# Kernel optimization log

Measured on AMD Instinct MI355X. Metric: run time of the kernel, lower is better.

The kernel has to match this reference:

```python
import jax, jax.numpy as jnp
import numpy as np
from jax import lax

N = 8192            # total ensemble boxes
W_IMG, H_IMG = 1920.0, 1080.0
NUM_MODELS = 5
CLUSTER_IOU = 0.5   # coalesce_boxes threshold


def setup_inputs() -> dict:
    key = jax.random.key(0)
    k1, k2, k3, k4, k5 = jax.random.split(key, 5)
    x1 = jax.random.uniform(k1, (N,)) * (W_IMG - 60.0)
    y1 = jax.random.uniform(k2, (N,)) * (H_IMG - 60.0)
    w = jax.random.uniform(k3, (N,)) * 180.0 + 4.0
    h = jax.random.uniform(k4, (N,)) * 180.0 + 4.0
    boxes = jnp.stack([x1, y1, x1 + w, y1 + h], axis=1)          # [N,4] xyxy
    scores = jax.random.uniform(k5, (N,)) * 0.7 + 0.3            # conf_thres=0.3
    return {"boxes": boxes, "scores": scores, "num_models": NUM_MODELS}


def _edf_forward(boxes, scores, num_models):
    n = boxes.shape[0]
    # clip to image (original also rounds; rounding omitted to keep grads alive)
    x1 = jnp.clip(boxes[:, 0], 0.0, W_IMG)
    y1 = jnp.clip(boxes[:, 1], 0.0, H_IMG)
    x2 = jnp.clip(boxes[:, 2], 0.0, W_IMG)
    y2 = jnp.clip(boxes[:, 3], 0.0, H_IMG)
    # coalesce_boxes processes boxes in descending score order (sort asc, pop)
    order = jnp.argsort(-scores)
    b = jnp.stack([x1, y1, x2, y2], axis=1)[order]               # [N,4]
    s = scores[order]
    bx1, by1, bx2, by2 = b[:, 0], b[:, 1], b[:, 2], b[:, 3]
    area = (bx2 - bx1 + 1.0) * (by2 - by1 + 1.0)
    # pairwise IoU with the +1 convention of bb_intersection_over_union
    ix1 = jnp.maximum(bx1[:, None], bx1[None, :])
    iy1 = jnp.maximum(by1[:, None], by1[None, :])
    ix2 = jnp.minimum(bx2[:, None], bx2[None, :])
    iy2 = jnp.minimum(by2[:, None], by2[None, :])
    inter = jnp.maximum(ix2 - ix1 + 1.0, 0.0) * jnp.maximum(iy2 - iy1 + 1.0, 0.0)
    iou = inter / (area[:, None] + area[None, :] - inter)        # [N,N]
    adj = iou > CLUSTER_IOU
    # greedy clustering: in score order, an unassigned box becomes a cluster
    # head and absorbs every still-unassigned box with IoU(head, j) > 0.5
    def step(cluster, i):
        is_head = cluster[i] < 0
        cluster = jnp.where(is_head & (cluster < 0) & adj[i], i, cluster)
        return cluster, None
    cluster, _ = lax.scan(step, jnp.full((n,), -1, jnp.int32),
                          jnp.arange(n, dtype=jnp.int32))
    counts = jax.ops.segment_sum(jnp.ones((n,), jnp.float32), cluster, num_segments=n)
    # per-group nms() only returns pick[0]: the member with max y2 (ties -> first)
    seg_y2 = jax.ops.segment_max(by2, cluster, num_segments=n)
    idx = jnp.arange(n)
    cand = by2 >= seg_y2[cluster]
    first = jax.ops.segment_min(jnp.where(cand, idx, n), cluster, num_segments=n)
    is_pick = idx == first[cluster]
    # probFinal = sum of group scores; final score = probFinal / num_models
    prob = jax.ops.segment_sum(s, cluster, num_segments=n)
    score_out = prob[cluster] / num_models
    # 'consensus': keep group iff its size >= num_models / 3
    valid = counts >= (num_models / 3.0)
    keep = is_pick & valid[cluster]
    out = jnp.where(keep[:, None],
                    jnp.concatenate([b, score_out[:, None]], axis=1),
                    0.0)                                         # [N,5] padded
    return out, keep


def reference(boxes, scores, num_models):
    return _edf_forward(boxes, scores, num_models)
```

## Files before the change

### kernel.cpp

```cpp
#include <hip/hip_runtime.h>
#include <cstdint>

#define N 8192
#define NT 128
#define NROUNDS 6
typedef unsigned long long u64;
typedef unsigned int u32;

__device__ inline u64 readlane64(u64 v, int lane) {
  u32 lo = (u32)__builtin_amdgcn_readlane((int)(u32)v, lane);
  u32 hi = (u32)__builtin_amdgcn_readlane((int)(u32)(v >> 32), lane);
  return ((u64)hi << 32) | lo;
}

__global__ __launch_bounds__(256) void k_rank0(const float* __restrict__ scores,
                                               const float* __restrict__ boxes,
                                               float* __restrict__ bx1s, float* __restrict__ by1s,
                                               float* __restrict__ bx2s, float* __restrict__ by2s,
                                               float* __restrict__ ss, float* __restrict__ areas,
                                               int* __restrict__ cnt,
                                               float* __restrict__ prob,
                                               u64* __restrict__ y2f,
                                               u64* __restrict__ D,
                                               u64* __restrict__ S) {
#pragma clang fp contract(off)
  __shared__ u64 tile[1024];
  __shared__ int red[8][32];
  int t = threadIdx.x;
  int s = t >> 5, ei = t & 31;
  int e = blockIdx.x * 32 + ei;
  u64 ke = ((u64)__float_as_uint(scores[e]) << 32) | (u32)(0xFFFFFFFFu - (u32)e);
  int c = 0;
  for (int j0 = 0; j0 < N; j0 += 1024) {
    __syncthreads();
    for (int q = t; q < 1024; q += 256) {
      int j = j0 + q;
      tile[q] = ((u64)__float_as_uint(scores[j]) << 32) | (u32)(0xFFFFFFFFu - (u32)j);
    }
    __syncthreads();
    int k0 = s * 128;
#pragma unroll 8
    for (int k = 0; k < 128; ++k) c += (tile[k0 + k] > ke) ? 1 : 0;
  }
  red[s][ei] = c;
  __syncthreads();
  if (t < 32) {
    int r = 0;
#pragma unroll
    for (int q = 0; q < 8; ++q) r += red[q][t];
    int i = blockIdx.x * 32 + t;
    float x1 = fminf(fmaxf(boxes[i * 4 + 0], 0.0f), 1920.0f);
    float y1 = fminf(fmaxf(boxes[i * 4 + 1], 0.0f), 1080.0f);
    float x2 = fminf(fmaxf(boxes[i * 4 + 2], 0.0f), 1920.0f);
    float y2 = fminf(fmaxf(boxes[i * 4 + 3], 0.0f), 1080.0f);
    bx1s[r] = x1; by1s[r] = y1; bx2s[r] = x2; by2s[r] = y2;
    ss[r] = scores[i];
    areas[r] = (x2 - x1 + 1.0f) * (y2 - y1 + 1.0f);
    cnt[i] = 0; prob[i] = 0.0f; y2f[i] = 0ull;
  }
  if (blockIdx.x == 0) {
    if (t < NT) D[t] = 0ull;
    else if (t < 2 * NT) S[t - NT] = 0ull;
  }
}

__global__ __launch_bounds__(256) void k_adj(const float* __restrict__ bx1s, const float* __restrict__ by1s,
                                             const float* __restrict__ bx2s, const float* __restrict__ by2s,
                                             const float* __restrict__ areas,
                                             u64* __restrict__ mtile) {
#pragma clang fp contract(off)
  __shared__ float jx1[4][64], jy1[4][64], jx2[4][64], jy2[4][64], ja[4][64];
  int w = threadIdx.x >> 6, l = threadIdx.x & 63;
  int p = blockIdx.x * 4 + w;
  int gy = (int)((sqrtf(8.0f * (float)p + 1.0f) - 1.0f) * 0.5f);
  while ((gy + 1) * (gy + 2) / 2 <= p) ++gy;
  while (gy * (gy + 1) / 2 > p) --gy;
  int gx = p - gy * (gy + 1) / 2;

  int j = gx * 64 + l;
  jx1[w][l] = bx1s[j]; jy1[w][l] = by1s[j]; jx2[w][l] = bx2s[j]; jy2[w][l] = by2s[j]; ja[w][l] = areas[j];
  __syncthreads();
  int i = gy * 64 + l;
  float x1 = bx1s[i], y1 = by1s[i], x2 = bx2s[i], y2 = by2s[i], ai = areas[i];
  u64 bits = 0;
#pragma unroll 4
  for (int jj = 0; jj < 64; ++jj) {
    float ix1 = fmaxf(x1, jx1[w][jj]);
    float iy1 = fmaxf(y1, jy1[w][jj]);
    float ix2 = fminf(x2, jx2[w][jj]);
    float iy2 = fminf(y2, jy2[w][jj]);
    float iw = fmaxf(ix2 - ix1 + 1.0f, 0.0f);
    float ih = fmaxf(iy2 - iy1 + 1.0f, 0.0f);
    float inter = iw * ih;
    float uni = (ai + ja[w][jj]) - inter;
    float t = inter + inter;
    bool gt = t > uni;
    bool amb = fabsf(t - uni) <= 1e-6f * uni;
    if (__ballot(amb) != 0ull) {
      float iou = inter / uni;
      if (amb) gt = iou > 0.5f;
    }
    bits |= ((u64)gt) << jj;
  }
  mtile[((size_t)gy * NT + gx) * 64 + l] = bits;
  if (gx != gy) {
    u64 tb = 0;
#pragma unroll 8
    for (int c = 0; c < 64; ++c) {
      u64 wb = __ballot((bits >> c) & 1ull);
      tb = (l == c) ? wb : tb;
    }
    mtile[((size_t)gx * NT + gy) * 64 + l] = tb;
  }
}

__global__ __launch_bounds__(256) void k_round(const u64* __restrict__ mtile,
                                               u64* __restrict__ D,
                                               u64* __restrict__ S) {
  __shared__ u64 Dl[NT], Sl[NT];
  __shared__ u64 bw[3][4];
  int gy = blockIdx.x;
  int t = threadIdx.x;
  int w = t >> 6, r = t & 63;
  if (t < NT) Dl[t] = D[t];
  else Sl[t - NT] = S[t - NT];
  __syncthreads();
  u64 classified = Dl[gy] | Sl[gy];
  if (classified == ~0ull) return;
  bool unk = !((classified >> r) & 1ull);
  u64 anyD = 0, anyU = 0, anyE = 0;
  if (unk) {
    int k0 = 32 * w, k1 = min(k0 + 32, gy + 1);
    for (int k = k0; k < k1; ++k) {
      u64 m = mtile[((size_t)gy * NT + k) * 64 + r];
      if (k == gy) {
        m &= (1ull << r) - 1ull;
        anyD |= m & Dl[k];
        anyU |= m & ~Sl[k];
      } else {
        anyD |= m & Dl[k];
        anyU |= m & ~Sl[k];
        anyE |= m & ~(Sl[k] | Dl[k]);
      }
    }
  }
  u64 bD = __ballot(anyD != 0ull), bU = __ballot(anyU != 0ull), bE = __ballot(anyE != 0ull);
  if (r == 0) { bw[0][w] = bD; bw[1][w] = bU; bw[2][w] = bE; }
  __syncthreads();
  u64 rD = bw[0][0] | bw[0][1] | bw[0][2] | bw[0][3];
  u64 rU = bw[1][0] | bw[1][1] | bw[1][2] | bw[1][3];
  u64 rE = bw[2][0] | bw[2][1] | bw[2][2] | bw[2][3];
  u64 unkb = ~classified;
  if (rE == 0ull) {
    if (w == 0) {
      u64 dAA = mtile[((size_t)gy * NT + gy) * 64 + r];
      u64 heads = 0, todo = unkb & ~rD;
      while (todo) {
        int i = __builtin_ctzll(todo);
        heads |= 1ull << i;
        todo &= ~readlane64(dAA, i);
      }
      if (r == 0) {
        if (heads) atomicOr(&D[gy], heads);
        u64 ns = unkb & ~heads;
        if (ns) atomicOr(&S[gy], ns);
      }
    }
    return;
  }
  if (t == 0) {
    u64 newS = unkb & rD;
    u64 newD = unkb & ~rD & ~rU;
    if (newS) atomicOr(&S[gy], newS);
    if (newD) atomicOr(&D[gy], newD);
  }
}

__global__ __launch_bounds__(64, 1) void k_fix(const u64* __restrict__ mtile,
                                               u64* __restrict__ D,
                                               const u64* __restrict__ S) {
  __shared__ int ulist[N];
  int l = threadIdx.x;
  u64 D0 = D[l], D1 = D[64 + l];
  u64 S0 = S[l], S1 = S[64 + l];
  u64 u0 = ~(D0 | S0), u1 = ~(D1 | S1);
  int c0 = __popcll(u0), c1 = __popcll(u1);
  int p0 = c0, p1 = c1;
  for (int d = 1; d < 64; d <<= 1) {
    int v0 = __shfl_up(p0, d), v1 = __shfl_up(p1, d);
    if (l >= d) { p0 += v0; p1 += v1; }
  }
  int t0 = __shfl(p0, 63);
  int M = t0 + __shfl(p1, 63);
  {
    int o = p0 - c0;
    u64 v = u0;
    while (v) { int b = __builtin_ctzll(v); v &= v - 1; ulist[o++] = l * 64 + b; }
    o = t0 + p1 - c1;
    v = u1;
    while (v) { int b = __builtin_ctzll(v); v &= v - 1; ulist[o++] = (64 + l) * 64 + b; }
  }
  __syncthreads();
  if (M > 0) {
    u64 rx[8], ry[8];
    int pj[8];
    auto fetch = [&](int q, int j) {
      pj[q] = j;
      int jt = j >> 6, jl = j & 63;
      rx[q] = mtile[((size_t)jt * NT + l) * 64 + jl];
      ry[q] = mtile[((size_t)jt * NT + 64 + l) * 64 + jl];
    };
#pragma unroll
    for (int q = 0; q < 8; ++q) fetch(q, ulist[q < M ? q : M - 1]);
    for (int m = 0; m < M; ++m) {
      int slot = m & 7;
      int j = pj[slot];
      u64 vx = rx[slot], vy = ry[slot];
      int jt = j >> 6;
      u64 bm = (1ull << (j & 63)) - 1ull;
      u64 m0 = (l < jt) ? ~0ull : ((l == jt) ? bm : 0ull);
      u64 m1 = (64 + l < jt) ? ~0ull : ((64 + l == jt) ? bm : 0ull);
      bool hit = ((vx & D0 & m0) | (vy & D1 & m1)) != 0ull;
      bool head = (__ballot(hit) == 0ull);
      u64 bset = 1ull << (j & 63);
      D0 |= (head && (l == jt)) ? bset : 0ull;
      D1 |= (head && (64 + l == jt)) ? bset : 0ull;
      int nm = m + 8;
      fetch(slot, ulist[nm < M ? nm : M - 1]);
    }
  }
  D[l] = D0;
  D[64 + l] = D1;
}

__global__ __launch_bounds__(256) void k_cluster(const u64* __restrict__ mtile,
                                                 const u64* __restrict__ D,
                                                 const float* __restrict__ ss,
                                                 const float* __restrict__ by2s,
                                                 int* __restrict__ cluster,
                                                 int* __restrict__ cnt,
                                                 float* __restrict__ prob,
                                                 u64* __restrict__ y2f) {
  __shared__ u64 hlds[NT];
  __shared__ int red[4][64];
  int gy = blockIdx.x;
  if (threadIdx.x < NT) hlds[threadIdx.x] = D[threadIdx.x];
  __syncthreads();
  int w = threadIdx.x >> 6, r = threadIdx.x & 63;
  int best = 0x7fffffff;
  for (int kk = 0; kk < 32; ++kk) {
    int k = 32 * w + kk;
    u64 v = mtile[((size_t)gy * NT + k) * 64 + r] & hlds[k];
    if (v && best == 0x7fffffff) best = k * 64 + __builtin_ctzll(v);
  }
  red[w][r] = best;
  __syncthreads();
  if (w == 0) {
    int b = min(min(red[0][r], red[1][r]), min(red[2][r], red[3][r]));
    int j = gy * 64 + r;
    cluster[j] = b;
    atomicAdd(&cnt[b], 1);
    atomicAdd(&prob[b], ss[j]);
    u64 key = ((u64)__float_as_uint(by2s[j]) << 32) | (u32)(0xFFFFFFFFu - (u32)j);
    atomicMax(&y2f[b], key);
  }
}

__global__ __launch_bounds__(256) void k_out(const int* __restrict__ cluster,
                                             const float* __restrict__ bx1s, const float* __restrict__ by1s,
                                             const float* __restrict__ bx2s, const float* __restrict__ by2s,
                                             const int* __restrict__ cnt,
                                             const float* __restrict__ prob,
                                             const u64* __restrict__ y2f,
                                             const int* __restrict__ num_models,
                                             float* __restrict__ out) {
  int j = blockIdx.x * 256 + threadIdx.x;
  if (j >= N) return;
  int c = cluster[j];
  int nm = num_models[0];
  bool valid = (float)cnt[c] >= (float)nm / 3.0f;
  int jf = (int)(0xFFFFFFFFu - (u32)(y2f[c] & 0xFFFFFFFFull));
  bool keep = (jf == j) && valid;
  float o0 = 0.f, o1 = 0.f, o2 = 0.f, o3 = 0.f, o4 = 0.f;
  if (keep) {
    o0 = bx1s[j]; o1 = by1s[j]; o2 = bx2s[j]; o3 = by2s[j];
    o4 = prob[c] / (float)nm;
  }
  out[j * 5 + 0] = o0;
  out[j * 5 + 1] = o1;
  out[j * 5 + 2] = o2;
  out[j * 5 + 3] = o3;
  out[j * 5 + 4] = o4;
  out[N * 5 + j] = keep ? 1.0f : 0.0f;
}

extern "C" void kernel_launch(void* const* d_in, const int* in_sizes, int n_in,
                              void* d_out, int out_size, void* d_ws, size_t ws_size,
                              hipStream_t stream) {
  const float* boxes = (const float*)d_in[0];
  const float* scores = (const float*)d_in[1];
  const int* num_models = (const int*)d_in[2];
  float* out = (float*)d_out;

  char* p = (char*)d_ws;
  auto take = [&](size_t bytes) {
    char* r = p;
    p += (bytes + 255) & ~(size_t)255;
    return r;
  };
  float* bx1s = (float*)take((size_t)N * 4);
  float* by1s = (float*)take((size_t)N * 4);
  float* bx2s = (float*)take((size_t)N * 4);
  float* by2s = (float*)take((size_t)N * 4);
  float* ss   = (float*)take((size_t)N * 4);
  float* areas= (float*)take((size_t)N * 4);
  int* cluster= (int*)take((size_t)N * 4);
  int* cnt    = (int*)take((size_t)N * 4);
  float* prob = (float*)take((size_t)N * 4);
  u64* y2f    = (u64*)take((size_t)N * 8);
  u64* D      = (u64*)take((size_t)NT * 8);
  u64* S      = (u64*)take((size_t)NT * 8);
  u64* mtile  = (u64*)take((size_t)NT * NT * 64 * 8);

  k_rank0<<<N / 32, 256, 0, stream>>>(scores, boxes, bx1s, by1s, bx2s, by2s, ss, areas,
                                      cnt, prob, y2f, D, S);
  k_adj<<<NT * (NT + 1) / 2 / 4, 256, 0, stream>>>(bx1s, by1s, bx2s, by2s, areas, mtile);
  for (int r = 0; r < NROUNDS; ++r)
    k_round<<<NT, 256, 0, stream>>>(mtile, D, S);
  k_fix<<<1, 64, 0, stream>>>(mtile, D, S);
  k_cluster<<<N / 64, 256, 0, stream>>>(mtile, D, ss, by2s, cluster, cnt, prob, y2f);
  k_out<<<N / 256, 256, 0, stream>>>(cluster, bx1s, by1s, bx2s, by2s, cnt, prob, y2f, num_models, out);
}
```

Measured before the change: 177.7 us.

## Fuse all stages into one cooperative persistent kernel with grid syncs

Replaces the eleven separate kernel launches (rank, adjacency, six rounds, fix, cluster, output) with a single cooperative kernel of 256 blocks that separates the stages with grid.sync. Shared-memory tiles in the adjacency stage are replaced by wave shuffles, and the adjacency work loops over the triangular tile list persistently. This removes per-launch overhead and inter-kernel gaps. In exchange, the grid is limited to 256 blocks, which lowers parallelism in the adjacency stage, adds grid-barrier costs, and makes the single-wave fix step stall the whole grid.

```diff
diff --git a/kernel.cpp b/kernel.cpp
--- a/kernel.cpp
+++ b/kernel.cpp
@@ -1,5 +1,8 @@
 #include <hip/hip_runtime.h>
+#include <hip/hip_cooperative_groups.h>
 #include <cstdint>
+
+namespace cg = cooperative_groups;
 
 #define N 8192
 #define NT 128
@@ -7,291 +10,303 @@
 typedef unsigned long long u64;
 typedef unsigned int u32;
 
+#define OFF_BX1 (size_t)0
+#define OFF_BY1 (size_t)32768
+#define OFF_BX2 (size_t)65536
+#define OFF_BY2 (size_t)98304
+#define OFF_SS  (size_t)131072
+#define OFF_AR  (size_t)163840
+#define OFF_CL  (size_t)196608
+#define OFF_CNT (size_t)229376
+#define OFF_PRB (size_t)262144
+#define OFF_Y2F (size_t)294912
+#define OFF_D   (size_t)360448
+#define OFF_S   (size_t)361472
+#define OFF_MT  (size_t)362752
+
 __device__ inline u64 readlane64(u64 v, int lane) {
   u32 lo = (u32)__builtin_amdgcn_readlane((int)(u32)v, lane);
   u32 hi = (u32)__builtin_amdgcn_readlane((int)(u32)(v >> 32), lane);
   return ((u64)hi << 32) | lo;
 }
 
-__global__ __launch_bounds__(256) void k_rank0(const float* __restrict__ scores,
-                                               const float* __restrict__ boxes,
-                                               float* __restrict__ bx1s, float* __restrict__ by1s,
-                                               float* __restrict__ bx2s, float* __restrict__ by2s,
-                                               float* __restrict__ ss, float* __restrict__ areas,
-                                               int* __restrict__ cnt,
-                                               float* __restrict__ prob,
-                                               u64* __restrict__ y2f,
-                                               u64* __restrict__ D,
-                                               u64* __restrict__ S) {
+struct SmA { u64 tile[1024]; int red[8][32]; };
+struct SmC { u64 Dl[NT]; u64 Sl[NT]; u64 bw[3][4]; };
+struct SmD { int ulist[N]; };
+struct SmE { u64 hlds[NT]; int red2[4][64]; };
+union SmU { SmA a; SmC c; SmD d; SmE e; };
+
+__global__ __launch_bounds__(256, 1) void k_mega(const float* __restrict__ boxes,
+                                                 const float* __restrict__ scores,
+                                                 const int* __restrict__ num_models,
+                                                 float* __restrict__ out,
+                                                 char* __restrict__ ws) {
 #pragma clang fp contract(off)
-  __shared__ u64 tile[1024];
-  __shared__ int red[8][32];
-  int t = threadIdx.x;
-  int s = t >> 5, ei = t & 31;
-  int e = blockIdx.x * 32 + ei;
-  u64 ke = ((u64)__float_as_uint(scores[e]) << 32) | (u32)(0xFFFFFFFFu - (u32)e);
-  int c = 0;
-  for (int j0 = 0; j0 < N; j0 += 1024) {
-    __syncthreads();
-    for (int q = t; q < 1024; q += 256) {
-      int j = j0 + q;
-      tile[q] = ((u64)__float_as_uint(scores[j]) << 32) | (u32)(0xFFFFFFFFu - (u32)j);
-    }
-    __syncthreads();
-    int k0 = s * 128;
+  __shared__ SmU sm;
+  cg::grid_group grid = cg::this_grid();
+
+  float* bx1s  = (float*)(ws + OFF_BX1);
+  float* by1s  = (float*)(ws + OFF_BY1);
+  float* bx2s  = (float*)(ws + OFF_BX2);
+  float* by2s  = (float*)(ws + OFF_BY2);
+  float* ss    = (float*)(ws + OFF_SS);
+  float* areas = (float*)(ws + OFF_AR);
+  int* cluster = (int*)(ws + OFF_CL);
+  int* cnt     = (int*)(ws + OFF_CNT);
+  float* prob  = (float*)(ws + OFF_PRB);
+  u64* y2f     = (u64*)(ws + OFF_Y2F);
+  u64* D       = (u64*)(ws + OFF_D);
+  u64* S       = (u64*)(ws + OFF_S);
+  u64* mtile   = (u64*)(ws + OFF_MT);
+
+  const int t = threadIdx.x;
+  const int b = blockIdx.x;
+  const int w = t >> 6, l = t & 63;
+
+  {
+    int s = t >> 5, ei = t & 31;
+    int e = b * 32 + ei;
+    u64 ke = ((u64)__float_as_uint(scores[e]) << 32) | (u32)(0xFFFFFFFFu - (u32)e);
+    int c = 0;
+    for (int j0 = 0; j0 < N; j0 += 1024) {
+      __syncthreads();
+      for (int q = t; q < 1024; q += 256) {
+        int j = j0 + q;
+        sm.a.tile[q] = ((u64)__float_as_uint(scores[j]) << 32) | (u32)(0xFFFFFFFFu - (u32)j);
+      }
+      __syncthreads();
+      int k0 = s * 128;
 #pragma unroll 8
-    for (int k = 0; k < 128; ++k) c += (tile[k0 + k] > ke) ? 1 : 0;
-  }
-  red[s][ei] = c;
+      for (int k = 0; k < 128; ++k) c += (sm.a.tile[k0 + k] > ke) ? 1 : 0;
+    }
+    sm.a.red[s][ei] = c;
+    __syncthreads();
+    if (t < 32) {
+      int r = 0;
+#pragma unroll
+      for (int q = 0; q < 8; ++q) r += sm.a.red[q][t];
+      int i = b * 32 + t;
+      float x1 = fminf(fmaxf(boxes[i * 4 + 0], 0.0f), 1920.0f);
+      float y1 = fminf(fmaxf(boxes[i * 4 + 1], 0.0f), 1080.0f);
+      float x2 = fminf(fmaxf(boxes[i * 4 + 2], 0.0f), 1920.0f);
+      float y2 = fminf(fmaxf(boxes[i * 4 + 3], 0.0f), 1080.0f);
+      bx1s[r] = x1; by1s[r] = y1; bx2s[r] = x2; by2s[r] = y2;
+      ss[r] = scores[i];
+      areas[r] = (x2 - x1 + 1.0f) * (y2 - y1 + 1.0f);
+      cnt[i] = 0; prob[i] = 0.0f; y2f[i] = 0ull;
+    }
+    if (b == 0) {
+      if (t < NT) D[t] = 0ull;
+      else if (t < 2 * NT) S[t - NT] = 0ull;
+    }
+  }
+  __threadfence();
+  grid.sync();
+
+  {
+    const int NP = NT * (NT + 1) / 2;
+    for (int p = b * 4 + w; p < NP; p += 1024) {
+      int gy = (int)((sqrtf(8.0f * (float)p + 1.0f) - 1.0f) * 0.5f);
+      while ((gy + 1) * (gy + 2) / 2 <= p) ++gy;
+      while (gy * (gy + 1) / 2 > p) --gy;
+      int gx = p - gy * (gy + 1) / 2;
+      int j = gx * 64 + l, i = gy * 64 + l;
+      float jx1v = bx1s[j], jy1v = by1s[j], jx2v = bx2s[j], jy2v = by2s[j], jav = areas[j];
+      float x1 = bx1s[i], y1 = by1s[i], x2 = bx2s[i], y2 = by2s[i], ai = areas[i];
+      u64 bits = 0;
+#pragma unroll 4
+      for (int jj = 0; jj < 64; ++jj) {
+        float ix1 = fmaxf(x1, __shfl(jx1v, jj));
+        float iy1 = fmaxf(y1, __shfl(jy1v, jj));
+        float ix2 = fminf(x2, __shfl(jx2v, jj));
+        float iy2 = fminf(y2, __shfl(jy2v, jj));
+        float iw = fmaxf(ix2 - ix1 + 1.0f, 0.0f);
+        float ih = fmaxf(iy2 - iy1 + 1.0f, 0.0f);
+        float inter = iw * ih;
+        float uni = (ai + __shfl(jav, jj)) - inter;
+        float tt = inter + inter;
+        bool gt = tt > uni;
+        bool amb = fabsf(tt - uni) <= 1e-6f * uni;
+        if (__ballot(amb) != 0ull) {
+          float iou = inter / uni;
+          if (amb) gt = iou > 0.5f;
+        }
+        bits |= ((u64)gt) << jj;
+      }
+      mtile[((size_t)gy * NT + gx) * 64 + l] = bits;
+      if (gx != gy) {
+        u64 tb = 0;
+#pragma unroll 8
+        for (int cc = 0; cc < 64; ++cc) {
+          u64 wb = __ballot((bits >> cc) & 1ull);
+          tb = (l == cc) ? wb : tb;
+        }
+        mtile[((size_t)gx * NT + gy) * 64 + l] = tb;
+      }
+    }
+  }
+  __threadfence();
+  grid.sync();
+
+  for (int it = 0; it < NROUNDS; ++it) {
+    __syncthreads();
+    if (t < NT) sm.c.Dl[t] = D[t];
+    else sm.c.Sl[t - NT] = S[t - NT];
+    __syncthreads();
+    if (b < NT) {
+      int gy = b;
+      u64 classified = sm.c.Dl[gy] | sm.c.Sl[gy];
+      if (classified != ~0ull) {
+        bool unk = !((classified >> l) & 1ull);
+        u64 anyD = 0, anyU = 0, anyE = 0;
+        if (unk) {
+          int k0 = 32 * w, k1 = min(k0 + 32, gy + 1);
+          for (int k = k0; k < k1; ++k) {
+            u64 m = mtile[((size_t)gy * NT + k) * 64 + l];
+            if (k == gy) {
+              m &= (1ull << l) - 1ull;
+              anyD |= m & sm.c.Dl[k];
+              anyU |= m & ~sm.c.Sl[k];
+            } else {
+              anyD |= m & sm.c.Dl[k];
+              anyU |= m & ~sm.c.Sl[k];
+              anyE |= m & ~(sm.c.Sl[k] | sm.c.Dl[k]);
+            }
+          }
+        }
+        u64 bD = __ballot(anyD != 0ull), bU = __ballot(anyU != 0ull), bE = __ballot(anyE != 0ull);
+        if (l == 0) { sm.c.bw[0][w] = bD; sm.c.bw[1][w] = bU; sm.c.bw[2][w] = bE; }
+        __syncthreads();
+        u64 rD = sm.c.bw[0][0] | sm.c.bw[0][1] | sm.c.bw[0][2] | sm.c.bw[0][3];
+        u64 rU = sm.c.bw[1][0] | sm.c.bw[1][1] | sm.c.bw[1][2] | sm.c.bw[1][3];
+        u64 rE = sm.c.bw[2][0] | sm.c.bw[2][1] | sm.c.bw[2][2] | sm.c.bw[2][3];
+        u64 unkb = ~classified;
+        if (rE == 0ull) {
+          if (w == 0) {
+            u64 dAA = mtile[((size_t)gy * NT + gy) * 64 + l];
+            u64 heads = 0, todo = unkb & ~rD;
+            while (todo) {
+              int i2 = __builtin_ctzll(todo);
+              heads |= 1ull << i2;
+              todo &= ~readlane64(dAA, i2);
+            }
+            if (l == 0) {
+              if (heads) atomicOr(&D[gy], heads);
+              u64 ns = unkb & ~heads;
+              if (ns) atomicOr(&S[gy], ns);
+            }
+          }
+        } else if (t == 0) {
+          u64 newS = unkb & rD;
+          u64 newD2 = unkb & ~rD & ~rU;
+          if (newS) atomicOr(&S[gy], newS);
+          if (newD2) atomicOr(&D[gy], newD2);
+        }
+      }
+    }
+    __threadfence();
+    grid.sync();
+  }
+
   __syncthreads();
+  if (b == 0 && w == 0) {
+    u64 D0 = D[l], D1 = D[64 + l];
+    u64 S0 = S[l], S1 = S[64 + l];
+    u64 u0 = ~(D0 | S0), u1 = ~(D1 | S1);
+    int c0 = __popcll(u0), c1 = __popcll(u1);
+    int p0 = c0, p1 = c1;
+    for (int d2 = 1; d2 < 64; d2 <<= 1) {
+      int v0 = __shfl_up(p0, d2), v1 = __shfl_up(p1, d2);
+      if (l >= d2) { p0 += v0; p1 += v1; }
+    }
+    int t0s = __shfl(p0, 63);
+    int M = t0s + __shfl(p1, 63);
+    {
+      int o = p0 - c0; u64 v = u0;
+      while (v) { int bb = __builtin_ctzll(v); v &= v - 1; sm.d.ulist[o++] = l * 64 + bb; }
+      o = t0s + p1 - c1; v = u1;
+      while (v) { int bb = __builtin_ctzll(v); v &= v - 1; sm.d.ulist[o++] = (64 + l) * 64 + bb; }
+    }
+    asm volatile("s_waitcnt lgkmcnt(0)" ::: "memory");
+    if (M > 0) {
+      u64 rx[8], ry[8];
+      int pj[8];
+      auto fetch = [&](int q, int j) {
+        pj[q] = j;
+        int jt = j >> 6, jl = j & 63;
+        rx[q] = mtile[((size_t)jt * NT + l) * 64 + jl];
+        ry[q] = mtile[((size_t)jt * NT + 64 + l) * 64 + jl];
+      };
+#pragma unroll
+      for (int q = 0; q < 8; ++q) fetch(q, sm.d.ulist[q < M ? q : M - 1]);
+      for (int m = 0; m < M; ++m) {
+        int slot = m & 7;
+        int j = pj[slot];
+        u64 vx = rx[slot], vy = ry[slot];
+        int jt = j >> 6;
+        u64 bm = (1ull << (j & 63)) - 1ull;
+        u64 m0 = (l < jt) ? ~0ull : ((l == jt) ? bm : 0ull);
+        u64 m1 = (64 + l < jt) ? ~0ull : ((64 + l == jt) ? bm : 0ull);
+        bool hit = ((vx & D0 & m0) | (vy & D1 & m1)) != 0ull;
+        bool head = (__ballot(hit) == 0ull);
+        u64 bset = 1ull << (j & 63);
+        D0 |= (head && (l == jt)) ? bset : 0ull;
+        D1 |= (head && (64 + l == jt)) ? bset : 0ull;
+        int nm2 = m + 8;
+        fetch(slot, sm.d.ulist[nm2 < M ? nm2 : M - 1]);
+      }
+    }
+    D[l] = D0;
+    D[64 + l] = D1;
+  }
+  __threadfence();
+  grid.sync();
+
+  if (b < NT) {
+    __syncthreads();
+    if (t < NT) sm.e.hlds[t] = D[t];
+    __syncthreads();
+    int gy = b;
+    int best = 0x7fffffff;
+    for (int kk = 0; kk < 32; ++kk) {
+      int k = 32 * w + kk;
+      u64 v = mtile[((size_t)gy * NT + k) * 64 + l] & sm.e.hlds[k];
+      if (v && best == 0x7fffffff) best = k * 64 + __builtin_ctzll(v);
+    }
+    sm.e.red2[w][l] = best;
+    __syncthreads();
+    if (w == 0) {
+      int bb = min(min(sm.e.red2[0][l], sm.e.red2[1][l]), min(sm.e.red2[2][l], sm.e.red2[3][l]));
+      int j = gy * 64 + l;
+      cluster[j] = bb;
+      atomicAdd(&cnt[bb], 1);
+      atomicAdd(&prob[bb], ss[j]);
+      u64 key = ((u64)__float_as_uint(by2s[j]) << 32) | (u32)(0xFFFFFFFFu - (u32)j);
+      atomicMax(&y2f[bb], key);
+    }
+  }
+  __threadfence();
+  grid.sync();
+
   if (t < 32) {
-    int r = 0;
-#pragma unroll
-    for (int q = 0; q < 8; ++q) r += red[q][t];
-    int i = blockIdx.x * 32 + t;
-    float x1 = fminf(fmaxf(boxes[i * 4 + 0], 0.0f), 1920.0f);
-    float y1 = fminf(fmaxf(boxes[i * 4 + 1], 0.0f), 1080.0f);
-    float x2 = fminf(fmaxf(boxes[i * 4 + 2], 0.0f), 1920.0f);
-    float y2 = fminf(fmaxf(boxes[i * 4 + 3], 0.0f), 1080.0f);
-    bx1s[r] = x1; by1s[r] = y1; bx2s[r] = x2; by2s[r] = y2;
-    ss[r] = scores[i];
-    areas[r] = (x2 - x1 + 1.0f) * (y2 - y1 + 1.0f);
-    cnt[i] = 0; prob[i] = 0.0f; y2f[i] = 0ull;
-  }
-  if (blockIdx.x == 0) {
-    if (t < NT) D[t] = 0ull;
-    else if (t < 2 * NT) S[t - NT] = 0ull;
-  }
-}
-
-__global__ __launch_bounds__(256) void k_adj(const float* __restrict__ bx1s, const float* __restrict__ by1s,
-                                             const float* __restrict__ bx2s, const float* __restrict__ by2s,
-                                             const float* __restrict__ areas,
-                                             u64* __restrict__ mtile) {
-#pragma clang fp contract(off)
-  __shared__ float jx1[4][64], jy1[4][64], jx2[4][64], jy2[4][64], ja[4][64];
-  int w = threadIdx.x >> 6, l = threadIdx.x & 63;
-  int p = blockIdx.x * 4 + w;
-  int gy = (int)((sqrtf(8.0f * (float)p + 1.0f) - 1.0f) * 0.5f);
-  while ((gy + 1) * (gy + 2) / 2 <= p) ++gy;
-  while (gy * (gy + 1) / 2 > p) --gy;
-  int gx = p - gy * (gy + 1) / 2;
-
-  int j = gx * 64 + l;
-  jx1[w][l] = bx1s[j]; jy1[w][l] = by1s[j]; jx2[w][l] = bx2s[j]; jy2[w][l] = by2s[j]; ja[w][l] = areas[j];
-  __syncthreads();
-  int i = gy * 64 + l;
-  float x1 = bx1s[i], y1 = by1s[i], x2 = bx2s[i], y2 = by2s[i], ai = areas[i];
-  u64 bits = 0;
-#pragma unroll 4
-  for (int jj = 0; jj < 64; ++jj) {
-    float ix1 = fmaxf(x1, jx1[w][jj]);
-    float iy1 = fmaxf(y1, jy1[w][jj]);
-    float ix2 = fminf(x2, jx2[w][jj]);
-    float iy2 = fminf(y2, jy2[w][jj]);
-    float iw = fmaxf(ix2 - ix1 + 1.0f, 0.0f);
-    float ih = fmaxf(iy2 - iy1 + 1.0f, 0.0f);
-    float inter = iw * ih;
-    float uni = (ai + ja[w][jj]) - inter;
-    float t = inter + inter;
-    bool gt = t > uni;
-    bool amb = fabsf(t - uni) <= 1e-6f * uni;
-    if (__ballot(amb) != 0ull) {
-      float iou = inter / uni;
-      if (amb) gt = iou > 0.5f;
-    }
-    bits |= ((u64)gt) << jj;
-  }
-  mtile[((size_t)gy * NT + gx) * 64 + l] = bits;
-  if (gx != gy) {
-    u64 tb = 0;
-#pragma unroll 8
-    for (int c = 0; c < 64; ++c) {
-      u64 wb = __ballot((bits >> c) & 1ull);
-      tb = (l == c) ? wb : tb;
-    }
-    mtile[((size_t)gx * NT + gy) * 64 + l] = tb;
-  }
-}
-
-__global__ __launch_bounds__(256) void k_round(const u64* __restrict__ mtile,
-                                               u64* __restrict__ D,
-                                               u64* __restrict__ S) {
-  __shared__ u64 Dl[NT], Sl[NT];
-  __shared__ u64 bw[3][4];
-  int gy = blockIdx.x;
-  int t = threadIdx.x;
-  int w = t >> 6, r = t & 63;
-  if (t < NT) Dl[t] = D[t];
-  else Sl[t - NT] = S[t - NT];
-  __syncthreads();
-  u64 classified = Dl[gy] | Sl[gy];
-  if (classified == ~0ull) return;
-  bool unk = !((classified >> r) & 1ull);
-  u64 anyD = 0, anyU = 0, anyE = 0;
-  if (unk) {
-    int k0 = 32 * w, k1 = min(k0 + 32, gy + 1);
-    for (int k = k0; k < k1; ++k) {
-      u64 m = mtile[((size_t)gy * NT + k) * 64 + r];
-      if (k == gy) {
-        m &= (1ull << r) - 1ull;
-        anyD |= m & Dl[k];
-        anyU |= m & ~Sl[k];
-      } else {
-        anyD |= m & Dl[k];
-        anyU |= m & ~Sl[k];
-        anyE |= m & ~(Sl[k] | Dl[k]);
-      }
-    }
-  }
-  u64 bD = __ballot(anyD != 0ull), bU = __ballot(anyU != 0ull), bE = __ballot(anyE != 0ull);
-  if (r == 0) { bw[0][w] = bD; bw[1][w] = bU; bw[2][w] = bE; }
-  __syncthreads();
-  u64 rD = bw[0][0] | bw[0][1] | bw[0][2] | bw[0][3];
-  u64 rU = bw[1][0] | bw[1][1] | bw[1][2] | bw[1][3];
-  u64 rE = bw[2][0] | bw[2][1] | bw[2][2] | bw[2][3];
-  u64 unkb = ~classified;
-  if (rE == 0ull) {
-    if (w == 0) {
-      u64 dAA = mtile[((size_t)gy * NT + gy) * 64 + r];
-      u64 heads = 0, todo = unkb & ~rD;
-      while (todo) {
-        int i = __builtin_ctzll(todo);
-        heads |= 1ull << i;
-        todo &= ~readlane64(dAA, i);
-      }
-      if (r == 0) {
-        if (heads) atomicOr(&D[gy], heads);
-        u64 ns = unkb & ~heads;
-        if (ns) atomicOr(&S[gy], ns);
-      }
-    }
-    return;
-  }
-  if (t == 0) {
-    u64 newS = unkb & rD;
-    u64 newD = unkb & ~rD & ~rU;
-    if (newS) atomicOr(&S[gy], newS);
-    if (newD) atomicOr(&D[gy], newD);
-  }
-}
-
-__global__ __launch_bounds__(64, 1) void k_fix(const u64* __restrict__ mtile,
-                                               u64* __restrict__ D,
-                                               const u64* __restrict__ S) {
-  __shared__ int ulist[N];
-  int l = threadIdx.x;
-  u64 D0 = D[l], D1 = D[64 + l];
-  u64 S0 = S[l], S1 = S[64 + l];
-  u64 u0 = ~(D0 | S0), u1 = ~(D1 | S1);
-  int c0 = __popcll(u0), c1 = __popcll(u1);
-  int p0 = c0, p1 = c1;
-  for (int d = 1; d < 64; d <<= 1) {
-    int v0 = __shfl_up(p0, d), v1 = __shfl_up(p1, d);
-    if (l >= d) { p0 += v0; p1 += v1; }
-  }
-  int t0 = __shfl(p0, 63);
-  int M = t0 + __shfl(p1, 63);
-  {
-    int o = p0 - c0;
-    u64 v = u0;
-    while (v) { int b = __builtin_ctzll(v); v &= v - 1; ulist[o++] = l * 64 + b; }
-    o = t0 + p1 - c1;
-    v = u1;
-    while (v) { int b = __builtin_ctzll(v); v &= v - 1; ulist[o++] = (64 + l) * 64 + b; }
-  }
-  __syncthreads();
-  if (M > 0) {
-    u64 rx[8], ry[8];
-    int pj[8];
-    auto fetch = [&](int q, int j) {
-      pj[q] = j;
-      int jt = j >> 6, jl = j & 63;
-      rx[q] = mtile[((size_t)jt * NT + l) * 64 + jl];
-      ry[q] = mtile[((size_t)jt * NT + 64 + l) * 64 + jl];
-    };
-#pragma unroll
-    for (int q = 0; q < 8; ++q) fetch(q, ulist[q < M ? q : M - 1]);
-    for (int m = 0; m < M; ++m) {
-      int slot = m & 7;
-      int j = pj[slot];
-      u64 vx = rx[slot], vy = ry[slot];
-      int jt = j >> 6;
-      u64 bm = (1ull << (j & 63)) - 1ull;
-      u64 m0 = (l < jt) ? ~0ull : ((l == jt) ? bm : 0ull);
-      u64 m1 = (64 + l < jt) ? ~0ull : ((64 + l == jt) ? bm : 0ull);
-      bool hit = ((vx & D0 & m0) | (vy & D1 & m1)) != 0ull;
-      bool head = (__ballot(hit) == 0ull);
-      u64 bset = 1ull << (j & 63);
-      D0 |= (head && (l == jt)) ? bset : 0ull;
-      D1 |= (head && (64 + l == jt)) ? bset : 0ull;
-      int nm = m + 8;
-      fetch(slot, ulist[nm < M ? nm : M - 1]);
-    }
-  }
-  D[l] = D0;
-  D[64 + l] = D1;
-}
-
-__global__ __launch_bounds__(256) void k_cluster(const u64* __restrict__ mtile,
-                                                 const u64* __restrict__ D,
-                                                 const float* __restrict__ ss,
-                                                 const float* __restrict__ by2s,
-                                                 int* __restrict__ cluster,
-                                                 int* __restrict__ cnt,
-                                                 float* __restrict__ prob,
-                                                 u64* __restrict__ y2f) {
-  __shared__ u64 hlds[NT];
-  __shared__ int red[4][64];
-  int gy = blockIdx.x;
-  if (threadIdx.x < NT) hlds[threadIdx.x] = D[threadIdx.x];
-  __syncthreads();
-  int w = threadIdx.x >> 6, r = threadIdx.x & 63;
-  int best = 0x7fffffff;
-  for (int kk = 0; kk < 32; ++kk) {
-    int k = 32 * w + kk;
-    u64 v = mtile[((size_t)gy * NT + k) * 64 + r] & hlds[k];
-    if (v && best == 0x7fffffff) best = k * 64 + __builtin_ctzll(v);
-  }
-  red[w][r] = best;
-  __syncthreads();
-  if (w == 0) {
-    int b = min(min(red[0][r], red[1][r]), min(red[2][r], red[3][r]));
-    int j = gy * 64 + r;
-    cluster[j] = b;
-    atomicAdd(&cnt[b], 1);
-    atomicAdd(&prob[b], ss[j]);
-    u64 key = ((u64)__float_as_uint(by2s[j]) << 32) | (u32)(0xFFFFFFFFu - (u32)j);
-    atomicMax(&y2f[b], key);
-  }
-}
-
-__global__ __launch_bounds__(256) void k_out(const int* __restrict__ cluster,
-                                             const float* __restrict__ bx1s, const float* __restrict__ by1s,
-                                             const float* __restrict__ bx2s, const float* __restrict__ by2s,
-                                             const int* __restrict__ cnt,
-                                             const float* __restrict__ prob,
-                                             const u64* __restrict__ y2f,
-                                             const int* __restrict__ num_models,
-                                             float* __restrict__ out) {
-  int j = blockIdx.x * 256 + threadIdx.x;
-  if (j >= N) return;
-  int c = cluster[j];
-  int nm = num_models[0];
-  bool valid = (float)cnt[c] >= (float)nm / 3.0f;
-  int jf = (int)(0xFFFFFFFFu - (u32)(y2f[c] & 0xFFFFFFFFull));
-  bool keep = (jf == j) && valid;
-  float o0 = 0.f, o1 = 0.f, o2 = 0.f, o3 = 0.f, o4 = 0.f;
-  if (keep) {
-    o0 = bx1s[j]; o1 = by1s[j]; o2 = bx2s[j]; o3 = by2s[j];
-    o4 = prob[c] / (float)nm;
-  }
-  out[j * 5 + 0] = o0;
-  out[j * 5 + 1] = o1;
-  out[j * 5 + 2] = o2;
-  out[j * 5 + 3] = o3;
-  out[j * 5 + 4] = o4;
-  out[N * 5 + j] = keep ? 1.0f : 0.0f;
+    int j = b * 32 + t;
+    int c = cluster[j];
+    int nm = num_models[0];
+    bool valid = (float)cnt[c] >= (float)nm / 3.0f;
+    int jf = (int)(0xFFFFFFFFu - (u32)(y2f[c] & 0xFFFFFFFFull));
+    bool keep = (jf == j) && valid;
+    float o0 = 0.f, o1 = 0.f, o2 = 0.f, o3 = 0.f, o4 = 0.f;
+    if (keep) {
+      o0 = bx1s[j]; o1 = by1s[j]; o2 = bx2s[j]; o3 = by2s[j];
+      o4 = prob[c] / (float)nm;
+    }
+    out[j * 5 + 0] = o0;
+    out[j * 5 + 1] = o1;
+    out[j * 5 + 2] = o2;
+    out[j * 5 + 3] = o3;
+    out[j * 5 + 4] = o4;
+    out[N * 5 + j] = keep ? 1.0f : 0.0f;
+  }
 }
 
 extern "C" void kernel_launch(void* const* d_in, const int* in_sizes, int n_in,
@@ -301,33 +316,10 @@
   const float* scores = (const float*)d_in[1];
   const int* num_models = (const int*)d_in[2];
   float* out = (float*)d_out;
-
-  char* p = (char*)d_ws;
-  auto take = [&](size_t bytes) {
-    char* r = p;
-    p += (bytes + 255) & ~(size_t)255;
-    return r;
-  };
-  float* bx1s = (float*)take((size_t)N * 4);
-  float* by1s = (float*)take((size_t)N * 4);
-  float* bx2s = (float*)take((size_t)N * 4);
-  float* by2s = (float*)take((size_t)N * 4);
-  float* ss   = (float*)take((size_t)N * 4);
-  float* areas= (float*)take((size_t)N * 4);
-  int* cluster= (int*)take((size_t)N * 4);
-  int* cnt    = (int*)take((size_t)N * 4);
-  float* prob = (float*)take((size_t)N * 4);
-  u64* y2f    = (u64*)take((size_t)N * 8);
-  u64* D      = (u64*)take((size_t)NT * 8);
-  u64* S      = (u64*)take((size_t)NT * 8);
-  u64* mtile  = (u64*)take((size_t)NT * NT * 64 * 8);
-
-  k_rank0<<<N / 32, 256, 0, stream>>>(scores, boxes, bx1s, by1s, bx2s, by2s, ss, areas,
-                                      cnt, prob, y2f, D, S);
-  k_adj<<<NT * (NT + 1) / 2 / 4, 256, 0, stream>>>(bx1s, by1s, bx2s, by2s, areas, mtile);
-  for (int r = 0; r < NROUNDS; ++r)
-    k_round<<<NT, 256, 0, stream>>>(mtile, D, S);
-  k_fix<<<1, 64, 0, stream>>>(mtile, D, S);
-  k_cluster<<<N / 64, 256, 0, stream>>>(mtile, D, ss, by2s, cluster, cnt, prob, y2f);
-  k_out<<<N / 256, 256, 0, stream>>>(cluster, bx1s, by1s, bx2s, by2s, cnt, prob, y2f, num_models, out);
+  char* ws = (char*)d_ws;
+
+  void* args[] = {(void*)&boxes, (void*)&scores, (void*)&num_models,
+                  (void*)&out, (void*)&ws};
+  hipLaunchCooperativeKernel((const void*)k_mega, dim3(256), dim3(256),
+                             args, 0, stream);
 }
```

Result: slower. 709.0 us (+299.0%).

## Drop transposed adjacency writes and merge final clustering round with fix pass

Applied to the files above, without the earlier changes.

The adjacency kernel now writes only the lower-triangular tiles and no longer builds transposed copies with 64 ballots per tile. The cluster-assignment kernel scans only tiles up to its own diagonal, masking the diagonal tile to include self, since a cluster head always precedes its members in score order. The number of separate round launches drops to four, and the last round runs in the same launch as the serial fix pass, which is placed in an extra block. That block may read D and S while other blocks are still updating them, relying on the fix pass to resolve any bits it sees as unclassified.

```diff
diff --git a/kernel.cpp b/kernel.cpp
--- a/kernel.cpp
+++ b/kernel.cpp
@@ -3,7 +3,7 @@
 
 #define N 8192
 #define NT 128
-#define NROUNDS 6
+#define NPLAIN 4
 typedef unsigned long long u64;
 typedef unsigned int u32;
 
@@ -103,64 +103,54 @@
     bits |= ((u64)gt) << jj;
   }
   mtile[((size_t)gy * NT + gx) * 64 + l] = bits;
-  if (gx != gy) {
-    u64 tb = 0;
-#pragma unroll 8
-    for (int c = 0; c < 64; ++c) {
-      u64 wb = __ballot((bits >> c) & 1ull);
-      tb = (l == c) ? wb : tb;
-    }
-    mtile[((size_t)gx * NT + gy) * 64 + l] = tb;
-  }
-}
-
-__global__ __launch_bounds__(256) void k_round(const u64* __restrict__ mtile,
-                                               u64* __restrict__ D,
-                                               u64* __restrict__ S) {
-  __shared__ u64 Dl[NT], Sl[NT];
-  __shared__ u64 bw[3][4];
-  int gy = blockIdx.x;
+}
+
+struct SmC { u64 Dl[NT]; u64 Sl[NT]; u64 bw[3][4]; };
+
+__device__ inline void round_body(const u64* __restrict__ mtile,
+                                  u64* __restrict__ D, u64* __restrict__ S,
+                                  SmC& sm, int gy) {
   int t = threadIdx.x;
-  int w = t >> 6, r = t & 63;
-  if (t < NT) Dl[t] = D[t];
-  else Sl[t - NT] = S[t - NT];
-  __syncthreads();
-  u64 classified = Dl[gy] | Sl[gy];
+  int w = t >> 6, l = t & 63;
+  if (t < NT) sm.Dl[t] = D[t];
+  else sm.Sl[t - NT] = S[t - NT];
+  __syncthreads();
+  u64 classified = sm.Dl[gy] | sm.Sl[gy];
   if (classified == ~0ull) return;
-  bool unk = !((classified >> r) & 1ull);
+  bool unk = !((classified >> l) & 1ull);
   u64 anyD = 0, anyU = 0, anyE = 0;
   if (unk) {
     int k0 = 32 * w, k1 = min(k0 + 32, gy + 1);
     for (int k = k0; k < k1; ++k) {
-      u64 m = mtile[((size_t)gy * NT + k) * 64 + r];
+      u64 m = mtile[((size_t)gy * NT + k) * 64 + l];
       if (k == gy) {
-        m &= (1ull << r) - 1ull;
-        anyD |= m & Dl[k];
-        anyU |= m & ~Sl[k];
+        m &= (1ull << l) - 1ull;
+        anyD |= m & sm.Dl[k];
+        anyU |= m & ~sm.Sl[k];
       } else {
-        anyD |= m & Dl[k];
-        anyU |= m & ~Sl[k];
-        anyE |= m & ~(Sl[k] | Dl[k]);
+        anyD |= m & sm.Dl[k];
+        anyU |= m & ~sm.Sl[k];
+        anyE |= m & ~(sm.Sl[k] | sm.Dl[k]);
       }
     }
   }
   u64 bD = __ballot(anyD != 0ull), bU = __ballot(anyU != 0ull), bE = __ballot(anyE != 0ull);
-  if (r == 0) { bw[0][w] = bD; bw[1][w] = bU; bw[2][w] = bE; }
-  __syncthreads();
-  u64 rD = bw[0][0] | bw[0][1] | bw[0][2] | bw[0][3];
-  u64 rU = bw[1][0] | bw[1][1] | bw[1][2] | bw[1][3];
-  u64 rE = bw[2][0] | bw[2][1] | bw[2][2] | bw[2][3];
+  if (l == 0) { sm.bw[0][w] = bD; sm.bw[1][w] = bU; sm.bw[2][w] = bE; }
+  __syncthreads();
+  u64 rD = sm.bw[0][0] | sm.bw[0][1] | sm.bw[0][2] | sm.bw[0][3];
+  u64 rU = sm.bw[1][0] | sm.bw[1][1] | sm.bw[1][2] | sm.bw[1][3];
+  u64 rE = sm.bw[2][0] | sm.bw[2][1] | sm.bw[2][2] | sm.bw[2][3];
   u64 unkb = ~classified;
   if (rE == 0ull) {
     if (w == 0) {
-      u64 dAA = mtile[((size_t)gy * NT + gy) * 64 + r];
+      u64 dAA = mtile[((size_t)gy * NT + gy) * 64 + l];
       u64 heads = 0, todo = unkb & ~rD;
       while (todo) {
         int i = __builtin_ctzll(todo);
         heads |= 1ull << i;
         todo &= ~readlane64(dAA, i);
       }
-      if (r == 0) {
+      if (l == 0) {
         if (heads) atomicOr(&D[gy], heads);
         u64 ns = unkb & ~heads;
         if (ns) atomicOr(&S[gy], ns);
@@ -176,10 +166,23 @@
   }
 }
 
-__global__ __launch_bounds__(64, 1) void k_fix(const u64* __restrict__ mtile,
+__global__ __launch_bounds__(256) void k_round(const u64* __restrict__ mtile,
                                                u64* __restrict__ D,
-                                               const u64* __restrict__ S) {
-  __shared__ int ulist[N];
+                                               u64* __restrict__ S) {
+  __shared__ SmC sm;
+  round_body(mtile, D, S, sm, blockIdx.x);
+}
+
+struct SmF { int ulist[N]; };
+union SmRF { SmC c; SmF f; };
+
+__global__ __launch_bounds__(256) void k_roundfix(const u64* __restrict__ mtile,
+                                                  u64* __restrict__ D,
+                                                  u64* __restrict__ S) {
+  __shared__ SmRF sm;
+  int b = blockIdx.x;
+  if (b < NT) { round_body(mtile, D, S, sm.c, b); return; }
+  if (threadIdx.x >= 64) return;
   int l = threadIdx.x;
   u64 D0 = D[l], D1 = D[64 + l];
   u64 S0 = S[l], S1 = S[64 + l];
@@ -193,14 +196,12 @@
   int t0 = __shfl(p0, 63);
   int M = t0 + __shfl(p1, 63);
   {
-    int o = p0 - c0;
-    u64 v = u0;
-    while (v) { int b = __builtin_ctzll(v); v &= v - 1; ulist[o++] = l * 64 + b; }
-    o = t0 + p1 - c1;
-    v = u1;
-    while (v) { int b = __builtin_ctzll(v); v &= v - 1; ulist[o++] = (64 + l) * 64 + b; }
-  }
-  __syncthreads();
+    int o = p0 - c0; u64 v = u0;
+    while (v) { int bb = __builtin_ctzll(v); v &= v - 1; sm.f.ulist[o++] = l * 64 + bb; }
+    o = t0 + p1 - c1; v = u1;
+    while (v) { int bb = __builtin_ctzll(v); v &= v - 1; sm.f.ulist[o++] = (64 + l) * 64 + bb; }
+  }
+  asm volatile("s_waitcnt lgkmcnt(0)" ::: "memory");
   if (M > 0) {
     u64 rx[8], ry[8];
     int pj[8];
@@ -211,7 +212,7 @@
       ry[q] = mtile[((size_t)jt * NT + 64 + l) * 64 + jl];
     };
 #pragma unroll
-    for (int q = 0; q < 8; ++q) fetch(q, ulist[q < M ? q : M - 1]);
+    for (int q = 0; q < 8; ++q) fetch(q, sm.f.ulist[q < M ? q : M - 1]);
     for (int m = 0; m < M; ++m) {
       int slot = m & 7;
       int j = pj[slot];
@@ -226,7 +227,7 @@
       D0 |= (head && (l == jt)) ? bset : 0ull;
       D1 |= (head && (64 + l == jt)) ? bset : 0ull;
       int nm = m + 8;
-      fetch(slot, ulist[nm < M ? nm : M - 1]);
+      fetch(slot, sm.f.ulist[nm < M ? nm : M - 1]);
     }
   }
   D[l] = D0;
@@ -246,18 +247,21 @@
   int gy = blockIdx.x;
   if (threadIdx.x < NT) hlds[threadIdx.x] = D[threadIdx.x];
   __syncthreads();
-  int w = threadIdx.x >> 6, r = threadIdx.x & 63;
+  int w = threadIdx.x >> 6, l = threadIdx.x & 63;
   int best = 0x7fffffff;
   for (int kk = 0; kk < 32; ++kk) {
     int k = 32 * w + kk;
-    u64 v = mtile[((size_t)gy * NT + k) * 64 + r] & hlds[k];
+    if (k > gy) break;
+    u64 m = mtile[((size_t)gy * NT + k) * 64 + l];
+    if (k == gy) m &= (2ull << l) - 1ull;
+    u64 v = m & hlds[k];
     if (v && best == 0x7fffffff) best = k * 64 + __builtin_ctzll(v);
   }
-  red[w][r] = best;
+  red[w][l] = best;
   __syncthreads();
   if (w == 0) {
-    int b = min(min(red[0][r], red[1][r]), min(red[2][r], red[3][r]));
-    int j = gy * 64 + r;
+    int b = min(min(red[0][l], red[1][l]), min(red[2][l], red[3][l]));
+    int j = gy * 64 + l;
     cluster[j] = b;
     atomicAdd(&cnt[b], 1);
     atomicAdd(&prob[b], ss[j]);
@@ -324,10 +328,10 @@
 
   k_rank0<<<N / 32, 256, 0, stream>>>(scores, boxes, bx1s, by1s, bx2s, by2s, ss, areas,
                                       cnt, prob, y2f, D, S);
-  k_adj<<<NT * (NT + 1) / 2 / 4, 256, 0, stream>>>(bx1s, by1s, bx2s, by2s, areas, mtile);
-  for (int r = 0; r < NROUNDS; ++r)
+  k_adj<<<(NT * (NT + 1) / 2 + 3) / 4, 256, 0, stream>>>(bx1s, by1s, bx2s, by2s, areas, mtile);
+  for (int r = 0; r < NPLAIN; ++r)
     k_round<<<NT, 256, 0, stream>>>(mtile, D, S);
-  k_fix<<<1, 64, 0, stream>>>(mtile, D, S);
+  k_roundfix<<<NT + 1, 256, 0, stream>>>(mtile, D, S);
   k_cluster<<<N / 64, 256, 0, stream>>>(mtile, D, ss, by2s, cluster, cnt, prob, y2f);
   k_out<<<N / 256, 256, 0, stream>>>(cluster, bx1s, by1s, bx2s, by2s, cnt, prob, y2f, num_models, out);
 }
```

After: 191.9 us. 1.08x slower.
